# Kernel tuning notes

Hardware: AMD Instinct MI355X
Metric: run time of the kernel (lower is better)

## Reference

```python
import jax, jax.numpy as jnp
import numpy as np

UNITS = 256
GROUPS = 8
EPS = 1e-3  # keras GroupNormalization default epsilon


def group_norm(x, gamma, beta, groups=GROUPS, eps=EPS):
    # x: [B,H,W,C], normalize per group over (H,W,C//groups)
    B, H, W, C = x.shape
    xg = x.reshape(B, H, W, groups, C // groups)
    mean = xg.mean(axis=(1, 2, 4), keepdims=True)
    var = xg.var(axis=(1, 2, 4), keepdims=True)
    xn = (xg - mean) * jax.lax.rsqrt(var + eps)
    xn = xn.reshape(B, H, W, C)
    return xn * gamma + beta


def setup_inputs() -> dict:
    key = jax.random.key(0)
    ks = jax.random.split(key, 10)
    B, H, W, C = 4, 64, 64, UNITS
    s = 1.0 / np.sqrt(C)
    x = jax.random.normal(ks[0], (B, H, W, C), dtype=jnp.float32)
    return {
        "x": x,
        "gamma": jnp.ones((C,), jnp.float32),
        "beta": jnp.zeros((C,), jnp.float32),
        "Wq": jax.random.uniform(ks[1], (C, C), jnp.float32, -s, s),
        "bq": jnp.zeros((C,), jnp.float32),
        "Wk": jax.random.uniform(ks[2], (C, C), jnp.float32, -s, s),
        "bk": jnp.zeros((C,), jnp.float32),
        "Wv": jax.random.uniform(ks[3], (C, C), jnp.float32, -s, s),
        "bv": jnp.zeros((C,), jnp.float32),
        # proj kernel init scale ~0 -> near-zero weights; use tiny random for nontrivial grads
        "Wp": jax.random.uniform(ks[4], (C, C), jnp.float32, -1e-5, 1e-5),
        "bp": jnp.zeros((C,), jnp.float32),
    }


def reference(x, gamma, beta, Wq, bq, Wk, bk, Wv, bv, Wp, bp):
    B, H, W, C = x.shape
    scale = jnp.float32(C) ** -0.5
    xn = group_norm(x, gamma, beta)  # [B,H,W,C]
    n = H * W
    xf = xn.reshape(B, n, C)
    q = xf @ Wq + bq  # [B,N,C]
    k = xf @ Wk + bk
    v = xf @ Wv + bv
    attn = jnp.einsum('bnc,bmc->bnm', q, k) * scale  # [B,N,N]
    attn = jax.nn.softmax(attn, axis=-1)
    out = jnp.einsum('bnm,bmc->bnc', attn, v)  # [B,N,C]
    out = out @ Wp + bp
    # NOTE: original code reassigns `inputs = self.norm(inputs)` before the
    # residual, so the skip connection uses the NORMALIZED input.
    return xn + out.reshape(B, H, W, C)
```

## Files before the change

kernel.cpp:

```cpp
#include <hip/hip_runtime.h>
#include <hip/hip_bf16.h>

typedef unsigned short u16;
typedef unsigned char u8;
typedef short short8 __attribute__((ext_vector_type(8)));
typedef float floatx4 __attribute__((ext_vector_type(4)));
typedef int intx8 __attribute__((ext_vector_type(8)));
typedef long long i64;

#define BB 4
#define NN 4096
#define CC 256
#define NG 8
#define M_TOT (BB * NN)
#define GN_EPS 1e-3f
#define ATT_SCALE 0.0625f
#define MCONST 2.5f
#define UNIT_SCALE 0x7F7F7F7F

__device__ __forceinline__ u16 f2bf(float f) {
  __hip_bfloat16 h = __float2bfloat16(f);
  return __builtin_bit_cast(u16, h);
}
__device__ __forceinline__ float bf2f(u16 u) {
  unsigned int i = ((unsigned int)u) << 16;
  return __builtin_bit_cast(float, i);
}
__device__ __forceinline__ unsigned pack2(float a, float b) {
  return (unsigned)f2bf(a) | ((unsigned)f2bf(b) << 16);
}
__device__ __forceinline__ unsigned pk4f8(float a, float b, float c, float d) {
  unsigned v = __builtin_amdgcn_cvt_pk_fp8_f32(a, b, 0, false);
  v = __builtin_amdgcn_cvt_pk_fp8_f32(c, d, v, true);
  return v;
}
__device__ __forceinline__ u8 f8byte(float a) {
  return (u8)(__builtin_amdgcn_cvt_pk_fp8_f32(a, a, 0, false) & 0xFF);
}

typedef __attribute__((address_space(3))) unsigned int lds_u32;
typedef const __attribute__((address_space(1))) unsigned int glb_u32;
#define ASYNC16(g, l) \
  __builtin_amdgcn_global_load_lds((glb_u32*)(g), (lds_u32*)(l), 16, 0, 0)

__global__ void prep_stats(const float* __restrict__ x,
                           const float* __restrict__ Wq, const float* __restrict__ Wk,
                           const float* __restrict__ Wv, const float* __restrict__ Wp,
                           float* __restrict__ part,
                           u16* __restrict__ wqT, u16* __restrict__ wkT,
                           u16* __restrict__ wvT, u16* __restrict__ wpT) {
  __shared__ u16 Ts[64][68];
  int blk = blockIdx.x;
  int t = threadIdx.x;
  if (blk < 512) {
    int b = blk >> 7, chunk = blk & 127;
    const float* p = x + ((size_t)b * NN + chunk * 32) * CC + t;
    float s = 0.f, ss = 0.f;
    for (int i = 0; i < 32; ++i) { float v = p[(size_t)i * CC]; s += v; ss += v * v; }
    for (int off = 1; off < 32; off <<= 1) { s += __shfl_xor(s, off); ss += __shfl_xor(ss, off); }
    if ((t & 31) == 0) {
      int g = t >> 5;
      part[((size_t)blk * NG + g) * 2 + 0] = s;
      part[((size_t)blk * NG + g) * 2 + 1] = ss;
    }
  } else {
    int pid = blk - 512;
    int y = pid >> 4, tile = pid & 15;
    int o0 = (tile >> 2) * 64, c0 = (tile & 3) * 64;
    const float* W = (y == 0) ? Wq : (y == 1) ? Wk : (y == 2) ? Wv : Wp;
    u16* WT = (y == 0) ? wqT : (y == 1) ? wkT : (y == 2) ? wvT : wpT;
    int cl = t >> 4, o4 = t & 15;
    for (int it = 0; it < 4; ++it) {
      int c = cl + it * 16;
      float4 v = *reinterpret_cast<const float4*>(W + (size_t)(c0 + c) * CC + o0 + o4 * 4);
      Ts[c][o4 * 4 + 0] = f2bf(v.x); Ts[c][o4 * 4 + 1] = f2bf(v.y);
      Ts[c][o4 * 4 + 2] = f2bf(v.z); Ts[c][o4 * 4 + 3] = f2bf(v.w);
    }
    __syncthreads();
    int ol = t >> 3, c8 = t & 7;
    for (int it = 0; it < 2; ++it) {
      int o = ol + it * 32;
      uint4 uv;
      uv.x = (unsigned)Ts[c8 * 8 + 0][o] | ((unsigned)Ts[c8 * 8 + 1][o] << 16);
      uv.y = (unsigned)Ts[c8 * 8 + 2][o] | ((unsigned)Ts[c8 * 8 + 3][o] << 16);
      uv.z = (unsigned)Ts[c8 * 8 + 4][o] | ((unsigned)Ts[c8 * 8 + 5][o] << 16);
      uv.w = (unsigned)Ts[c8 * 8 + 6][o] | ((unsigned)Ts[c8 * 8 + 7][o] << 16);
      *reinterpret_cast<uint4*>(WT + (size_t)(o0 + o) * CC + c0 + c8 * 8) = uv;
    }
  }
}

__global__ __launch_bounds__(256) void gn_apply(
    const float* __restrict__ x, const float* __restrict__ gamma,
    const float* __restrict__ beta, const float* __restrict__ part,
    u16* __restrict__ xnb) {
  __shared__ float gnst[16];
  int blk = blockIdx.x;
  int t = threadIdx.x;
  int b = blk >> 7;
  if (t < 64) {
    int g = t >> 3, j = t & 7;
    float s = 0.f, ss = 0.f;
    for (int ch = j; ch < 128; ch += 8) {
      size_t idx = (((size_t)(b * 128 + ch)) * NG + g) * 2;
      s += part[idx]; ss += part[idx + 1];
    }
    for (int off = 1; off < 8; off <<= 1) { s += __shfl_xor(s, off); ss += __shfl_xor(ss, off); }
    if (j == 0) {
      const float cnt = (float)(NN * (CC / NG));
      float mean = s / cnt;
      float var = ss / cnt - mean * mean;
      gnst[g * 2] = mean;
      gnst[g * 2 + 1] = rsqrtf(var + GN_EPS);
    }
  }
  __syncthreads();
  int row0 = blk * 32;
#pragma unroll
  for (int it = 0; it < 8; ++it) {
    int idx = t + it * 256;
    int rl = idx >> 6, c4 = idx & 63;
    int g = c4 >> 3;
    float mean = gnst[g * 2], rstd = gnst[g * 2 + 1];
    size_t gidx = (size_t)(row0 + rl) * 64 + c4;
    float4 v = reinterpret_cast<const float4*>(x)[gidx];
    float4 gm = reinterpret_cast<const float4*>(gamma)[c4];
    float4 bt = reinterpret_cast<const float4*>(beta)[c4];
    ushort4 o;
    o.x = f2bf((v.x - mean) * rstd * gm.x + bt.x);
    o.y = f2bf((v.y - mean) * rstd * gm.y + bt.y);
    o.z = f2bf((v.z - mean) * rstd * gm.z + bt.z);
    o.w = f2bf((v.w - mean) * rstd * gm.w + bt.w);
    reinterpret_cast<ushort4*>(xnb)[gidx] = o;
  }
}

#define LDT 72
__global__ __launch_bounds__(256) void gemm_qkv(
    const u16* __restrict__ xnb,
    const u16* __restrict__ wqT, const u16* __restrict__ wkT, const u16* __restrict__ wvT,
    const float* __restrict__ bq, const float* __restrict__ bk, const float* __restrict__ bv,
    u8* __restrict__ qb, u8* __restrict__ kb, u8* __restrict__ vTb) {
  __shared__ u16 sm[2 * 128 * LDT];
  u16* Asp = sm;
  u16* Bsp = sm + 128 * LDT;
  int m0 = blockIdx.x * 128;
  int widx = blockIdx.y >> 1;
  int n0 = (blockIdx.y & 1) * 128;
  const u16* wT = (widx == 0) ? wqT : (widx == 1) ? wkT : wvT;
  const float* bias = (widx == 0) ? bq : (widx == 1) ? bk : bv;
  int t = threadIdx.x, w = t >> 6, lane = t & 63, lo = lane & 15, hi = lane >> 4;
  int wm = (w >> 1) * 64, wn = (w & 1) * 64;
  floatx4 acc[4][4];
  for (int i = 0; i < 4; ++i) for (int j = 0; j < 4; ++j) acc[i][j] = (floatx4){0.f, 0.f, 0.f, 0.f};
  for (int kt = 0; kt < 4; ++kt) {
    int k0 = kt * 64;
    __syncthreads();
    for (int i = 0; i < 4; ++i) {
      int idx = t + i * 256, r = idx >> 3, c8 = idx & 7;
      *reinterpret_cast<uint4*>(Asp + r * LDT + c8 * 8) =
          *reinterpret_cast<const uint4*>(xnb + (size_t)(m0 + r) * CC + k0 + c8 * 8);
      *reinterpret_cast<uint4*>(Bsp + r * LDT + c8 * 8) =
          *reinterpret_cast<const uint4*>(wT + (size_t)(n0 + r) * CC + k0 + c8 * 8);
    }
    __syncthreads();
    for (int k32 = 0; k32 < 2; ++k32) {
      short8 af[4], bfr[4];
      for (int mt = 0; mt < 4; ++mt)
        af[mt] = *reinterpret_cast<const short8*>(Asp + (wm + mt * 16 + lo) * LDT + k32 * 32 + hi * 8);
      for (int nt = 0; nt < 4; ++nt)
        bfr[nt] = *reinterpret_cast<const short8*>(Bsp + (wn + nt * 16 + lo) * LDT + k32 * 32 + hi * 8);
      for (int mt = 0; mt < 4; ++mt)
        for (int nt = 0; nt < 4; ++nt)
          acc[mt][nt] = __builtin_amdgcn_mfma_f32_16x16x32_bf16(af[mt], bfr[nt], acc[mt][nt], 0, 0, 0);
    }
  }
  __syncthreads();
  for (int mt = 0; mt < 4; ++mt)
    for (int nt = 0; nt < 4; ++nt)
      for (int r = 0; r < 4; ++r) {
        int rr = wm + mt * 16 + hi * 4 + r;
        int cc2 = wn + nt * 16 + lo;
        sm[rr * 130 + cc2] = f2bf(acc[mt][nt][r] + bias[n0 + cc2]);
      }
  __syncthreads();
  if (widx < 2) {
    u8* outp = (widx == 0) ? qb : kb;
    for (int j = 0; j < 8; ++j) {
      int c = t + j * 256;
      int row = c >> 4, chl = c & 15;
      const u16* sp = sm + row * 130 + chl * 8;
      uint2 val;
      val.x = pk4f8(bf2f(sp[0]), bf2f(sp[1]), bf2f(sp[2]), bf2f(sp[3]));
      val.y = pk4f8(bf2f(sp[4]), bf2f(sp[5]), bf2f(sp[6]), bf2f(sp[7]));
      int rowg = m0 + row;
      int chg = (n0 >> 3) + chl;
      *reinterpret_cast<uint2*>(outp + (size_t)rowg * CC + chg * 8) = val;
    }
  } else {
    int dloc = t & 127;
    int dglob = n0 + dloc;
    int bb = m0 >> 12, tk = m0 & (NN - 1);
    u8* dst = vTb + ((size_t)(bb * CC + dglob)) * NN + tk;
#pragma unroll
    for (int it = 0; it < 2; ++it) {
      int ub = (t >> 7) * 2 + it * 4;
      unsigned wds[8];
#pragma unroll
      for (int uo = 0; uo < 2; ++uo) {
        int u = ub + uo;
        int rbase = 64 * (u & 1) + 4 * (u >> 1);
#pragma unroll
        for (int q = 0; q < 4; ++q) {
          int r0 = rbase + q * 16;
          wds[uo * 4 + q] = pk4f8(bf2f(sm[(r0 + 0) * 130 + dloc]), bf2f(sm[(r0 + 1) * 130 + dloc]),
                                  bf2f(sm[(r0 + 2) * 130 + dloc]), bf2f(sm[(r0 + 3) * 130 + dloc]));
        }
      }
      *reinterpret_cast<uint4*>(dst + ub * 16) = (uint4){wds[0], wds[1], wds[2], wds[3]};
      *reinterpret_cast<uint4*>(dst + ub * 16 + 16) = (uint4){wds[4], wds[5], wds[6], wds[7]};
    }
  }
}

__global__ __launch_bounds__(256, 2) void fa_kernel(
    const u8* __restrict__ qb, const u8* __restrict__ kb, const u8* __restrict__ vTb,
    u8* __restrict__ Opart, float* __restrict__ Lpart, u16* __restrict__ aob, int S) {
  __shared__ u8 Ks[128 * 256];
  __shared__ u8 vTs[256 * 128];
  int by = blockIdx.y;
  int b = by / S, split = by - b * S;
  int t = threadIdx.x, w = t >> 6, lane = t & 63, lo = lane & 15, hi = lane >> 4;
  int qw = blockIdx.x * 64 + w * 16;

  intx8 qf[2];
  {
    const u8* qrow = qb + ((size_t)(b * NN + qw + lo)) * CC;
#pragma unroll
    for (int kk = 0; kk < 2; ++kk) {
      uint4 a0 = *reinterpret_cast<const uint4*>(qrow + kk * 128 + hi * 32);
      uint4 a1 = *reinterpret_cast<const uint4*>(qrow + kk * 128 + hi * 32 + 16);
      qf[kk] = (intx8){(int)a0.x, (int)a0.y, (int)a0.z, (int)a0.w,
                       (int)a1.x, (int)a1.y, (int)a1.z, (int)a1.w};
    }
  }
  floatx4 oacc[16];
#pragma unroll
  for (int dt = 0; dt < 16; ++dt) oacc[dt] = (floatx4){0.f, 0.f, 0.f, 0.f};
  float lacc = 0.f;

  const int TILES = NN / 128;
  int jt0 = split * (TILES / S), jt1 = jt0 + TILES / S;
  const u8* kb_b = kb + (size_t)b * NN * CC;
  const u8* vb_b = vTb + (size_t)b * CC * NN;

  for (int jt = jt0; jt < jt1; ++jt) {
    int j0 = jt * 128;
    __syncthreads();
#pragma unroll
    for (int i = 0; i < 8; ++i) {
      int base = w * 512 + i * 64;
      int sl = base + lane;
      int row = sl >> 4;
      int u = (sl & 15) ^ (row & 7);
      ASYNC16(kb_b + (size_t)(j0 + row) * CC + u * 16, Ks + base * 16);
    }
#pragma unroll
    for (int i = 0; i < 8; ++i) {
      int base = w * 512 + i * 64;
      int sl = base + lane;
      int d = sl >> 3;
      int u = (sl & 7) ^ (d & 7);
      ASYNC16(vb_b + (size_t)d * NN + j0 + u * 16, vTs + base * 16);
    }
    __syncthreads();

    int pAw[8];
#pragma unroll
    for (int g = 0; g < 8; ++g) {
      int row = g * 16 + lo;
      const u8* kr = Ks + row * 256;
      int rs = row & 7;
      floatx4 s = (floatx4){0.f, 0.f, 0.f, 0.f};
#pragma unroll
      for (int kk = 0; kk < 2; ++kk) {
        uint4 c0 = *reinterpret_cast<const uint4*>(kr + ((kk * 8 + hi * 2 + 0) ^ rs) * 16);
        uint4 c1 = *reinterpret_cast<const uint4*>(kr + ((kk * 8 + hi * 2 + 1) ^ rs) * 16);
        intx8 kf = (intx8){(int)c0.x, (int)c0.y, (int)c0.z, (int)c0.w,
                           (int)c1.x, (int)c1.y, (int)c1.z, (int)c1.w};
        s = __builtin_amdgcn_mfma_scale_f32_16x16x128_f8f6f4(
            kf, qf[kk], s, 0, 0, 0, UNIT_SCALE, 0, UNIT_SCALE);
      }
      float p0 = __expf(fmaf(s[0], ATT_SCALE, -MCONST));
      float p1 = __expf(fmaf(s[1], ATT_SCALE, -MCONST));
      float p2 = __expf(fmaf(s[2], ATT_SCALE, -MCONST));
      float p3 = __expf(fmaf(s[3], ATT_SCALE, -MCONST));
      lacc += (p0 + p1) + (p2 + p3);
      pAw[g] = (int)pk4f8(p0, p1, p2, p3);
    }
    intx8 pA = (intx8){pAw[0], pAw[1], pAw[2], pAw[3],
                       pAw[4], pAw[5], pAw[6], pAw[7]};

#pragma unroll
    for (int dt = 0; dt < 16; ++dt) {
      int d = dt * 16 + lo;
      const u8* vr = vTs + d * 128;
      int ds7 = d & 7;
      uint4 v0 = *reinterpret_cast<const uint4*>(vr + ((hi * 2 + 0) ^ ds7) * 16);
      uint4 v1 = *reinterpret_cast<const uint4*>(vr + ((hi * 2 + 1) ^ ds7) * 16);
      intx8 vf = (intx8){(int)v0.x, (int)v0.y, (int)v0.z, (int)v0.w,
                         (int)v1.x, (int)v1.y, (int)v1.z, (int)v1.w};
      oacc[dt] = __builtin_amdgcn_mfma_scale_f32_16x16x128_f8f6f4(
          pA, vf, oacc[dt], 0, 0, 0, UNIT_SCALE, 0, UNIT_SCALE);
    }
  }

  lacc += __shfl_xor(lacc, 16);
  lacc += __shfl_xor(lacc, 32);

  if (S == 1) {
    float inv[4];
#pragma unroll
    for (int r = 0; r < 4; ++r) inv[r] = 1.0f / __shfl(lacc, 4 * hi + r);
#pragma unroll
    for (int dt = 0; dt < 16; ++dt)
#pragma unroll
      for (int r = 0; r < 4; ++r) {
        size_t row = (size_t)(b * NN + qw + 4 * hi + r);
        aob[row * CC + dt * 16 + lo] = f2bf(oacc[dt][r] * inv[r]);
      }
  } else {
    if (hi == 0)
      Lpart[(size_t)split * M_TOT + b * NN + qw + lo] = lacc;
    u8* op = Opart + (size_t)split * M_TOT * CC;
#pragma unroll
    for (int dt = 0; dt < 16; ++dt)
#pragma unroll
      for (int r = 0; r < 4; ++r) {
        size_t row = (size_t)(b * NN + qw + 4 * hi + r);
        op[row * CC + dt * 16 + lo] = f8byte(oacc[dt][r]);
      }
  }
}

__global__ __launch_bounds__(256) void gemm_proj(
    const u16* __restrict__ aob, const u8* __restrict__ Opart,
    const float* __restrict__ Lpart,
    const u16* __restrict__ wpT, const float* __restrict__ bp,
    const u16* __restrict__ xnb, float* __restrict__ out, int S) {
  __shared__ u16 As[64 * LDT];
  __shared__ u16 Bs[128 * LDT];
  __shared__ float linv[64];
  int m0 = blockIdx.x * 64;
  int n0 = blockIdx.y * 128;
  int t = threadIdx.x, w = t >> 6, lane = t & 63, lo = lane & 15, hi = lane >> 4;
  int wm = (w >> 1) * 32, wn = (w & 1) * 64;
  if (S > 1 && t < 64) {
    float l = 0.f;
    for (int sp = 0; sp < S; ++sp) l += Lpart[(size_t)sp * M_TOT + m0 + t];
    linv[t] = 1.f / l;
  }
  floatx4 acc[2][4];
  for (int i = 0; i < 2; ++i) for (int j = 0; j < 4; ++j) acc[i][j] = (floatx4){0.f, 0.f, 0.f, 0.f};
  for (int kt = 0; kt < 4; ++kt) {
    int k0 = kt * 64;
    __syncthreads();
    for (int i = 0; i < 2; ++i) {
      int c = t + i * 256, r = c >> 3, c8 = c & 7;
      if (S == 1) {
        *reinterpret_cast<uint4*>(As + r * LDT + c8 * 8) =
            *reinterpret_cast<const uint4*>(aob + (size_t)(m0 + r) * CC + k0 + c8 * 8);
      } else {
        float f[8] = {0, 0, 0, 0, 0, 0, 0, 0};
        for (int sp = 0; sp < S; ++sp) {
          uint2 uv = *reinterpret_cast<const uint2*>(
              Opart + (size_t)sp * M_TOT * CC + (size_t)(m0 + r) * CC + k0 + c8 * 8);
          f[0] += __builtin_amdgcn_cvt_f32_fp8(uv.x, 0);
          f[1] += __builtin_amdgcn_cvt_f32_fp8(uv.x, 1);
          f[2] += __builtin_amdgcn_cvt_f32_fp8(uv.x, 2);
          f[3] += __builtin_amdgcn_cvt_f32_fp8(uv.x, 3);
          f[4] += __builtin_amdgcn_cvt_f32_fp8(uv.y, 0);
          f[5] += __builtin_amdgcn_cvt_f32_fp8(uv.y, 1);
          f[6] += __builtin_amdgcn_cvt_f32_fp8(uv.y, 2);
          f[7] += __builtin_amdgcn_cvt_f32_fp8(uv.y, 3);
        }
        float iv = linv[r];
        uint4 o;
        o.x = pack2(f[0] * iv, f[1] * iv); o.y = pack2(f[2] * iv, f[3] * iv);
        o.z = pack2(f[4] * iv, f[5] * iv); o.w = pack2(f[6] * iv, f[7] * iv);
        *reinterpret_cast<uint4*>(As + r * LDT + c8 * 8) = o;
      }
    }
    for (int i = 0; i < 4; ++i) {
      int c = t + i * 256, r = c >> 3, c8 = c & 7;
      *reinterpret_cast<uint4*>(Bs + r * LDT + c8 * 8) =
          *reinterpret_cast<const uint4*>(wpT + (size_t)(n0 + r) * CC + k0 + c8 * 8);
    }
    __syncthreads();
    for (int k32 = 0; k32 < 2; ++k32) {
      short8 af[2], bfr[4];
      for (int mt = 0; mt < 2; ++mt)
        af[mt] = *reinterpret_cast<const short8*>(As + (wm + mt * 16 + lo) * LDT + k32 * 32 + hi * 8);
      for (int nt = 0; nt < 4; ++nt)
        bfr[nt] = *reinterpret_cast<const short8*>(Bs + (wn + nt * 16 + lo) * LDT + k32 * 32 + hi * 8);
      for (int mt = 0; mt < 2; ++mt)
        for (int nt = 0; nt < 4; ++nt)
          acc[mt][nt] = __builtin_amdgcn_mfma_f32_16x16x32_bf16(af[mt], bfr[nt], acc[mt][nt], 0, 0, 0);
    }
  }
  for (int mt = 0; mt < 2; ++mt)
    for (int nt = 0; nt < 4; ++nt)
      for (int r = 0; r < 4; ++r) {
        int row = m0 + wm + mt * 16 + hi * 4 + r;
        int col = n0 + wn + nt * 16 + lo;
        size_t o = (size_t)row * CC + col;
        out[o] = acc[mt][nt][r] + bp[col] + bf2f(xnb[o]);
      }
}

extern "C" void kernel_launch(void* const* d_in, const int* in_sizes, int n_in,
                              void* d_out, int out_size, void* d_ws, size_t ws_size,
                              hipStream_t stream) {
  (void)in_sizes; (void)n_in; (void)out_size;
  const float* x     = (const float*)d_in[0];
  const float* gamma = (const float*)d_in[1];
  const float* beta  = (const float*)d_in[2];
  const float* Wq    = (const float*)d_in[3];
  const float* bq    = (const float*)d_in[4];
  const float* Wk    = (const float*)d_in[5];
  const float* bk    = (const float*)d_in[6];
  const float* Wv    = (const float*)d_in[7];
  const float* bv    = (const float*)d_in[8];
  const float* Wp    = (const float*)d_in[9];
  const float* bp    = (const float*)d_in[10];
  float* out = (float*)d_out;

  char* w = (char*)d_ws;
  float* part  = (float*)w;              w += 512 * NG * 2 * 4;
  const size_t SZ = (size_t)M_TOT * CC * 2;
  const size_t SZ8 = (size_t)M_TOT * CC;
  u16* xnb = (u16*)w; w += SZ;
  u8* qb   = (u8*)w;  w += SZ8;
  u8* kb   = (u8*)w;  w += SZ8;
  u8* vTb  = (u8*)w;  w += SZ8;
  u16* aob = (u16*)w; w += SZ;
  u16* wqT = (u16*)w; w += (size_t)CC * CC * 2;
  u16* wkT = (u16*)w; w += (size_t)CC * CC * 2;
  u16* wvT = (u16*)w; w += (size_t)CC * CC * 2;
  u16* wpT = (u16*)w; w += (size_t)CC * CC * 2;

  size_t used = (size_t)(w - (char*)d_ws);
  size_t per_split = SZ8 + (size_t)M_TOT * 4 + 256;
  int S = 2;
  if (used + 2 * per_split > ws_size) S = 1;
  u8* Opart = (u8*)w;                    w += (size_t)S * SZ8;
  float* Lpart = (float*)w;

  prep_stats<<<576, 256, 0, stream>>>(x, Wq, Wk, Wv, Wp, part, wqT, wkT, wvT, wpT);
  gn_apply<<<512, 256, 0, stream>>>(x, gamma, beta, part, xnb);
  gemm_qkv<<<dim3(M_TOT / 128, 6), 256, 0, stream>>>(xnb, wqT, wkT, wvT, bq, bk, bv, qb, kb, vTb);
  fa_kernel<<<dim3(NN / 64, BB * S), 256, 0, stream>>>(qb, kb, vTb, Opart, Lpart, aob, S);
  gemm_proj<<<dim3(M_TOT / 64, 2), 256, 0, stream>>>(aob, Opart, Lpart, wpT, bp, xnb, out, S);
}
```

Baseline: 174.5 us.

## Pipeline K/V tile loads in halves with vmcnt-gated waits in flash attention

Splits each 128-key K and V tile stage into two halves and issues the async loads for the next tile's halves as soon as the current half of shared memory has been consumed. Explicit s_waitcnt vmcnt counts and raw s_barriers replace the full __syncthreads pairs, so global loads overlap with the QK and PV MFMA work. This adds tightly coupled wait-count bookkeeping, and it depends on the exact number of outstanding loads per thread. Extra barriers per iteration could hurt if that overlap does not pay for them.

```diff
diff --git a/kernel.cpp b/kernel.cpp
--- a/kernel.cpp
+++ b/kernel.cpp
@@ -233,6 +233,11 @@
   int t = threadIdx.x, w = t >> 6, lane = t & 63, lo = lane & 15, hi = lane >> 4;
   int qw = blockIdx.x * 64 + w * 16;
 
+  const int TILES = NN / 128;
+  int jt0 = split * (TILES / S), jt1 = jt0 + TILES / S;
+  const u8* kb_b = kb + (size_t)b * NN * CC;
+  const u8* vb_b = vTb + (size_t)b * CC * NN;
+
   intx8 qf[2];
   {
     const u8* qrow = qb + ((size_t)(b * NN + qw + lo)) * CC;
@@ -244,40 +249,48 @@
                        (int)a1.x, (int)a1.y, (int)a1.z, (int)a1.w};
     }
   }
-  floatx4 oacc[16];
-#pragma unroll
-  for (int dt = 0; dt < 16; ++dt) oacc[dt] = (floatx4){0.f, 0.f, 0.f, 0.f};
-  float lacc = 0.f;
-
-  const int TILES = NN / 128;
-  int jt0 = split * (TILES / S), jt1 = jt0 + TILES / S;
-  const u8* kb_b = kb + (size_t)b * NN * CC;
-  const u8* vb_b = vTb + (size_t)b * CC * NN;
-
-  for (int jt = jt0; jt < jt1; ++jt) {
-    int j0 = jt * 128;
-    __syncthreads();
-#pragma unroll
-    for (int i = 0; i < 8; ++i) {
-      int base = w * 512 + i * 64;
+
+  auto STAGE_K = [&](int j0, int h) {
+#pragma unroll
+    for (int i = 0; i < 4; ++i) {
+      int base = h * 1024 + w * 256 + i * 64;
       int sl = base + lane;
       int row = sl >> 4;
       int u = (sl & 15) ^ (row & 7);
       ASYNC16(kb_b + (size_t)(j0 + row) * CC + u * 16, Ks + base * 16);
     }
-#pragma unroll
-    for (int i = 0; i < 8; ++i) {
-      int base = w * 512 + i * 64;
+  };
+  auto STAGE_V = [&](int j0, int h) {
+#pragma unroll
+    for (int i = 0; i < 4; ++i) {
+      int base = h * 1024 + w * 256 + i * 64;
       int sl = base + lane;
       int d = sl >> 3;
       int u = (sl & 7) ^ (d & 7);
       ASYNC16(vb_b + (size_t)d * NN + j0 + u * 16, vTs + base * 16);
     }
-    __syncthreads();
-
-    int pAw[8];
-#pragma unroll
-    for (int g = 0; g < 8; ++g) {
+  };
+
+  floatx4 oacc[16];
+#pragma unroll
+  for (int dt = 0; dt < 16; ++dt) oacc[dt] = (floatx4){0.f, 0.f, 0.f, 0.f};
+  float lacc = 0.f;
+
+  {
+    int j0 = jt0 * 128;
+    STAGE_K(j0, 0); STAGE_K(j0, 1); STAGE_V(j0, 0); STAGE_V(j0, 1);
+  }
+
+  int pAw[8];
+  for (int jt = jt0; jt < jt1; ++jt) {
+    bool pf = (jt + 1 < jt1);
+    int nj0 = (jt + 1) * 128;
+
+    asm volatile("s_waitcnt vmcnt(12)" ::: "memory");
+    __builtin_amdgcn_sched_barrier(0);
+    __builtin_amdgcn_s_barrier();
+#pragma unroll
+    for (int g = 0; g < 4; ++g) {
       int row = g * 16 + lo;
       const u8* kr = Ks + row * 256;
       int rs = row & 7;
@@ -298,11 +311,47 @@
       lacc += (p0 + p1) + (p2 + p3);
       pAw[g] = (int)pk4f8(p0, p1, p2, p3);
     }
+    __builtin_amdgcn_s_barrier();
+    if (pf) STAGE_K(nj0, 0);
+
+    if (pf) asm volatile("s_waitcnt vmcnt(12)" ::: "memory");
+    else    asm volatile("s_waitcnt vmcnt(8)" ::: "memory");
+    __builtin_amdgcn_sched_barrier(0);
+    __builtin_amdgcn_s_barrier();
+#pragma unroll
+    for (int g = 4; g < 8; ++g) {
+      int row = g * 16 + lo;
+      const u8* kr = Ks + row * 256;
+      int rs = row & 7;
+      floatx4 s = (floatx4){0.f, 0.f, 0.f, 0.f};
+#pragma unroll
+      for (int kk = 0; kk < 2; ++kk) {
+        uint4 c0 = *reinterpret_cast<const uint4*>(kr + ((kk * 8 + hi * 2 + 0) ^ rs) * 16);
+        uint4 c1 = *reinterpret_cast<const uint4*>(kr + ((kk * 8 + hi * 2 + 1) ^ rs) * 16);
+        intx8 kf = (intx8){(int)c0.x, (int)c0.y, (int)c0.z, (int)c0.w,
+                           (int)c1.x, (int)c1.y, (int)c1.z, (int)c1.w};
+        s = __builtin_amdgcn_mfma_scale_f32_16x16x128_f8f6f4(
+            kf, qf[kk], s, 0, 0, 0, UNIT_SCALE, 0, UNIT_SCALE);
+      }
+      float p0 = __expf(fmaf(s[0], ATT_SCALE, -MCONST));
+      float p1 = __expf(fmaf(s[1], ATT_SCALE, -MCONST));
+      float p2 = __expf(fmaf(s[2], ATT_SCALE, -MCONST));
+      float p3 = __expf(fmaf(s[3], ATT_SCALE, -MCONST));
+      lacc += (p0 + p1) + (p2 + p3);
+      pAw[g] = (int)pk4f8(p0, p1, p2, p3);
+    }
+    __builtin_amdgcn_s_barrier();
+    if (pf) STAGE_K(nj0, 1);
+
     intx8 pA = (intx8){pAw[0], pAw[1], pAw[2], pAw[3],
                        pAw[4], pAw[5], pAw[6], pAw[7]};
 
-#pragma unroll
-    for (int dt = 0; dt < 16; ++dt) {
+    if (pf) asm volatile("s_waitcnt vmcnt(12)" ::: "memory");
+    else    asm volatile("s_waitcnt vmcnt(4)" ::: "memory");
+    __builtin_amdgcn_sched_barrier(0);
+    __builtin_amdgcn_s_barrier();
+#pragma unroll
+    for (int dt = 0; dt < 8; ++dt) {
       int d = dt * 16 + lo;
       const u8* vr = vTs + d * 128;
       int ds7 = d & 7;
@@ -313,6 +362,27 @@
       oacc[dt] = __builtin_amdgcn_mfma_scale_f32_16x16x128_f8f6f4(
           pA, vf, oacc[dt], 0, 0, 0, UNIT_SCALE, 0, UNIT_SCALE);
     }
+    __builtin_amdgcn_s_barrier();
+    if (pf) STAGE_V(nj0, 0);
+
+    if (pf) asm volatile("s_waitcnt vmcnt(12)" ::: "memory");
+    else    asm volatile("s_waitcnt vmcnt(0)" ::: "memory");
+    __builtin_amdgcn_sched_barrier(0);
+    __builtin_amdgcn_s_barrier();
+#pragma unroll
+    for (int dt = 8; dt < 16; ++dt) {
+      int d = dt * 16 + lo;
+      const u8* vr = vTs + d * 128;
+      int ds7 = d & 7;
+      uint4 v0 = *reinterpret_cast<const uint4*>(vr + ((hi * 2 + 0) ^ ds7) * 16);
+      uint4 v1 = *reinterpret_cast<const uint4*>(vr + ((hi * 2 + 1) ^ ds7) * 16);
+      intx8 vf = (intx8){(int)v0.x, (int)v0.y, (int)v0.z, (int)v0.w,
+                         (int)v1.x, (int)v1.y, (int)v1.z, (int)v1.w};
+      oacc[dt] = __builtin_amdgcn_mfma_scale_f32_16x16x128_f8f6f4(
+          pA, vf, oacc[dt], 0, 0, 0, UNIT_SCALE, 0, UNIT_SCALE);
+    }
+    __builtin_amdgcn_s_barrier();
+    if (pf) STAGE_V(nj0, 1);
   }
 
   lacc += __shfl_xor(lacc, 16);
```

New measurement: 351.9 us. +101.6%, slower.
